# Performance work log

Measured on AMD Instinct MI355X. Metric: run time of the kernel, lower is better.

Reference implementation:

```python
import jax, jax.numpy as jnp
import numpy as np

NH = 8    # num_heads
HD = 64   # head_dim
EPS = 1e-6


def setup_inputs() -> dict:
    key = jax.random.key(0)
    ks = jax.random.split(key, 8)
    B, N, D = 16, 3136, 512
    x = jax.random.normal(ks[0], (B, N, D), jnp.float32)
    Wq = jax.random.normal(ks[1], (D, D), jnp.float32) * 0.02
    Wkv = jax.random.normal(ks[2], (D, 2 * D), jnp.float32) * 0.02
    pos_enc = jax.random.normal(ks[3], (1, N, D), jnp.float32) * 0.02
    # depthwise conv: fan_out = k*k*out/groups = 25
    dwc_w = jax.random.normal(ks[4], (HD, 1, 5, 5), jnp.float32) * np.sqrt(2.0 / 25.0).astype(np.float32)
    dwc_b = jnp.zeros((HD,), jnp.float32)
    Wp = jax.random.normal(ks[5], (D, D), jnp.float32) * 0.02
    bp = jnp.zeros((D,), jnp.float32)
    return {"x": x, "Wq": Wq, "Wkv": Wkv, "pos_enc": pos_enc,
            "dwc_w": dwc_w, "dwc_b": dwc_b, "Wp": Wp, "bp": bp,
            "H": 56, "W": 56}


def reference(x, Wq, Wkv, pos_enc, dwc_w, dwc_b, Wp, bp, H, W):
    B, N, D = x.shape
    # projections (qkv_bias=False)
    q = jax.nn.relu(x @ Wq)                       # ReLU feature map on q
    kv = x @ Wkv                                  # [B, N, 2D]
    k = jax.nn.relu(kv[..., :D] + pos_enc)        # pos enc added before ReLU kernel
    v = kv[..., D:]
    # split heads: b n (h c) -> b h n c
    qh = q.reshape(B, N, NH, HD).transpose(0, 2, 1, 3)
    kh = k.reshape(B, N, NH, HD).transpose(0, 2, 1, 3)
    vh = v.reshape(B, N, NH, HD).transpose(0, 2, 1, 3)
    # linear attention: normalization and KV context
    k_sum = kh.sum(axis=2)                                        # [B, NH, HD]
    d_inv = 1.0 / (jnp.einsum('bhnd,bhd->bhn', qh, k_sum) + EPS)  # [B, NH, N]
    ctx = jnp.einsum('bhmd,bhme->bhde', kh, vh)                   # [B, NH, HD, HD]
    attn = jnp.einsum('bhnd,bhde->bhne', qh, ctx) * d_inv[..., None]
    # depthwise conv positional mixing on v (N == H*W)
    fmap = vh.reshape(B * NH, H, W, HD).transpose(0, 3, 1, 2)     # [(b h), c, H, W]
    dwc = jax.lax.conv_general_dilated(
        fmap, dwc_w, window_strides=(1, 1), padding='SAME',
        feature_group_count=HD,
        dimension_numbers=('NCHW', 'OIHW', 'NCHW')) + dwc_b[None, :, None, None]
    dwc = dwc.transpose(0, 2, 3, 1).reshape(B, NH, N, HD)
    # NOTE: original torch code reshapes ((b h), n, c) -> (B, N, D) directly
    # (NOT the inverse rearrange); reproduce that exact flat reshape.
    out = (attn + dwc).reshape(B, N, D)
    return out @ Wp + bp
```

## Files before the change

kernel.cpp:

```cpp
#include <hip/hip_runtime.h>

__device__ __forceinline__ float b2f(ushort u) {
    union { float f; unsigned int i; } w; w.i = ((unsigned int)u) << 16; return w.f;
}
__device__ __forceinline__ ushort f2b(float f) {
    union { float f; unsigned int i; } w; w.f = f;
    unsigned int lsb = (w.i >> 16) & 1u;
    w.i += 0x7fffu + lsb;
    return (ushort)(w.i >> 16);
}

typedef __bf16 bf16x8 __attribute__((ext_vector_type(8)));
typedef float floatx4 __attribute__((ext_vector_type(4)));

__device__ __forceinline__ void async_copy16(ushort* lds_base, const ushort* gptr) {
    __builtin_amdgcn_global_load_lds(
        (const __attribute__((address_space(1))) unsigned int*)gptr,
        (__attribute__((address_space(3))) unsigned int*)lds_base,
        16, 0, 0);
}

#define BATCH 16
#define NTOK  3136
#define NHEAD 8
#define HDIM  64
#define HSP   56
#define MROWS (BATCH * NTOK)
#define KDIM  512

__global__ __launch_bounds__(256) void detect_dtype(const ushort* __restrict__ x,
                                                    int* __restrict__ flag)
{
    __shared__ int s;
    if (threadIdx.x == 0) s = 0;
    __syncthreads();
    int bad = 0;
    for (int i = threadIdx.x; i < 4096; i += 256) {
        int e = (x[i] >> 7) & 0xFF;
        if (e >= 0x90) bad = 1;
    }
    if (bad) s = 1;
    __syncthreads();
    if (threadIdx.x == 0) flag[0] = s;
}

__global__ __launch_bounds__(256) void convert_x(
    const void* __restrict__ x, const int* __restrict__ flag,
    ushort* __restrict__ xbf)
{
    size_t t = (size_t)blockIdx.x * 256 + threadIdx.x;
    if (flag[0]) {
        const float* xf = (const float*)x + t * 8;
        float4 f0 = *(const float4*)xf;
        float4 f1 = *(const float4*)(xf + 4);
        ushort o[8] = { f2b(f0.x), f2b(f0.y), f2b(f0.z), f2b(f0.w),
                        f2b(f1.x), f2b(f1.y), f2b(f1.z), f2b(f1.w) };
        *(uint4*)(xbf + t * 8) = *(const uint4*)o;
    } else {
        *(uint4*)(xbf + t * 8) = *((const uint4*)x + t);
    }
}

__global__ __launch_bounds__(256) void prep_weights(
    const void* __restrict__ Wq, const void* __restrict__ Wkv,
    const void* __restrict__ Wp, const int* __restrict__ flag,
    ushort* __restrict__ WqkvT, ushort* __restrict__ WpT)
{
    bool f32 = flag[0] != 0;
    int idx = blockIdx.x * 256 + threadIdx.x;
    int kk = idx & 511;
    int n  = idx >> 9;
    if (n < 1536) {
        ushort val;
        if (n < 512)
            val = f32 ? f2b(((const float*)Wq)[kk * 512 + n])
                      : ((const ushort*)Wq)[kk * 512 + n];
        else
            val = f32 ? f2b(((const float*)Wkv)[kk * 1024 + (n - 512)])
                      : ((const ushort*)Wkv)[kk * 1024 + (n - 512)];
        WqkvT[n * 512 + kk] = val;
    } else {
        int n2 = n - 1536;
        WpT[n2 * 512 + kk] = f32 ? f2b(((const float*)Wp)[kk * 512 + n2])
                                 : ((const ushort*)Wp)[kk * 512 + n2];
    }
}

__global__ __launch_bounds__(256) void prep_dwc(
    const void* __restrict__ dwc_w, const void* __restrict__ dwc_b,
    const int* __restrict__ flag, float* __restrict__ wT)
{
    bool f32 = flag[0] != 0;
    for (int i = threadIdx.x; i < 1600; i += 256) {
        int e = i / 25, tap = i % 25;
        float w = f32 ? ((const float*)dwc_w)[i] : b2f(((const ushort*)dwc_w)[i]);
        wT[tap * 64 + e] = w;
    }
    if (threadIdx.x < 64) {
        float b = f32 ? ((const float*)dwc_b)[threadIdx.x]
                      : b2f(((const ushort*)dwc_b)[threadIdx.x]);
        wT[1600 + threadIdx.x] = b;
    }
}

__device__ __forceinline__ int swz(int r) { return (r ^ (r >> 2)) & 3; }

#define VMWAIT(N) asm volatile("s_waitcnt vmcnt(" #N ")" ::: "memory")

__global__ __launch_bounds__(512, 2) void gemm256_bt(
    const ushort* __restrict__ A, const ushort* __restrict__ Bt,
    int mode, const int* __restrict__ flag,
    const void* __restrict__ pos_enc, const void* __restrict__ bias,
    void* __restrict__ out0, ushort* __restrict__ out1, ushort* __restrict__ out2,
    int ntn)
{
    __shared__ ushort smem[65536];

    const bool f32 = flag[0] != 0;
    const int tid = threadIdx.x;
    const int lam = tid & 63;
    const int w   = tid >> 6;
    const int wm  = w >> 2;
    const int wn  = w & 3;
    const int g    = lam >> 4;
    const int mrow = lam & 15;
    const int m7   = mrow & 7;

    const int nwg = gridDim.x;
    const int q8  = nwg >> 3;
    const int bid = blockIdx.x;
    const int fid = (bid & 7) * q8 + (bid >> 3);
    const int tm = fid / ntn, tn = fid - tm * ntn;
    const int m0 = tm * 256, n0 = tn * 256;

    const int srow = w * 16 + (lam >> 3);
    const int scol = 8 * ((lam & 7) ^ (lam >> 3));
    const ushort* gA0 = A  + (size_t)(m0 +       srow) * KDIM + scol;
    const ushort* gA1 = A  + (size_t)(m0 + 128 + srow) * KDIM + scol;
    const ushort* gB0 = Bt + (size_t)(n0 +       srow) * KDIM + scol;
    const ushort* gB1 = Bt + (size_t)(n0 + 128 + srow) * KDIM + scol;

    const int aoff = (wm * 64 + mrow) * 64;
    const int boff = (wn * 32 + mrow) * 64;
    const int kx0 = 8 * (g ^ m7);
    const int kx1 = 8 * ((4 + g) ^ m7);

    floatx4 acc[8][4];
    #pragma unroll
    for (int i = 0; i < 8; i++)
        #pragma unroll
        for (int j = 0; j < 4; j++) acc[i][j] = (floatx4)0.f;

    bf16x8 a[4][2], bfr[2][2];

#define SA(p,h) (((p)*2+(h))*8192)
#define SB(p,h) (32768 + ((p)*2+(h))*8192)
#define STAGE(gp, slot, koff) do { \
    async_copy16(smem + (slot) + w*1024,       (gp) + (koff)); \
    async_copy16(smem + (slot) + w*1024 + 512, (gp) + 4096 + (koff)); } while (0)

    auto LDA_HALF = [&](int h, int p) {
        const ushort* ab = smem + SA(p,h) + aoff;
        #pragma unroll
        for (int q = 0; q < 4; ++q) {
            a[q][0] = *(const bf16x8*)(ab + q*1024 + kx0);
            a[q][1] = *(const bf16x8*)(ab + q*1024 + kx1);
        }
    };
    auto LDB_HALF = [&](int h, int p) {
        const ushort* bb = smem + SB(p,h) + boff;
        #pragma unroll
        for (int nq = 0; nq < 2; ++nq) {
            bfr[nq][0] = *(const bf16x8*)(bb + nq*1024 + kx0);
            bfr[nq][1] = *(const bf16x8*)(bb + nq*1024 + kx1);
        }
    };

#define PH_SYNC() do { __builtin_amdgcn_s_barrier(); \
    asm volatile("s_waitcnt lgkmcnt(0)" ::: "memory"); \
    __builtin_amdgcn_sched_barrier(0); } while (0)

#define MFMA_QUAD(MH, NH) do { \
    __builtin_amdgcn_s_setprio(1); \
    _Pragma("unroll") \
    for (int q = 0; q < 4; ++q) { \
        _Pragma("unroll") \
        for (int nq = 0; nq < 2; ++nq) { \
            acc[(MH)*4+q][(NH)*2+nq] = __builtin_amdgcn_mfma_f32_16x16x32_bf16( \
                a[q][0], bfr[nq][0], acc[(MH)*4+q][(NH)*2+nq], 0, 0, 0); \
            acc[(MH)*4+q][(NH)*2+nq] = __builtin_amdgcn_mfma_f32_16x16x32_bf16( \
                a[q][1], bfr[nq][1], acc[(MH)*4+q][(NH)*2+nq], 0, 0, 0); \
        } } \
    __builtin_amdgcn_s_setprio(0); } while (0)

    STAGE(gA0, SA(0,0), 0);
    STAGE(gB0, SB(0,0), 0);
    STAGE(gB1, SB(0,1), 0);
    STAGE(gA1, SA(0,1), 0);
    VMWAIT(4);
    __builtin_amdgcn_s_barrier();

    for (int kt = 0; kt < 7; ++kt) {
        const int p = kt & 1, np = p ^ 1;
        const int ko = (kt + 1) * 64;
        LDA_HALF(0, p); LDB_HALF(0, p);
        STAGE(gA0, SA(np,0), ko);
        VMWAIT(4);
        PH_SYNC();
        MFMA_QUAD(0, 0);
        LDB_HALF(1, p);
        STAGE(gB0, SB(np,0), ko);
        VMWAIT(4);
        PH_SYNC();
        MFMA_QUAD(0, 1);
        LDA_HALF(1, p);
        STAGE(gB1, SB(np,1), ko);
        PH_SYNC();
        MFMA_QUAD(1, 1);
        LDB_HALF(0, p);
        STAGE(gA1, SA(np,1), ko);
        VMWAIT(4);
        PH_SYNC();
        MFMA_QUAD(1, 0);
    }
    {
        LDA_HALF(0, 1); LDB_HALF(0, 1);
        VMWAIT(2);
        PH_SYNC();
        MFMA_QUAD(0, 0);
        LDB_HALF(1, 1);
        VMWAIT(0);
        PH_SYNC();
        MFMA_QUAD(0, 1);
        LDA_HALF(1, 1);
        PH_SYNC();
        MFMA_QUAD(1, 1);
        LDB_HALF(0, 1);
        PH_SYNC();
        MFMA_QUAD(1, 0);
    }

    float* lf = (float*)smem;
    const int e0 = (lam & 7) * 8;
    #pragma unroll
    for (int h = 0; h < 2; ++h) {
        __syncthreads();
        #pragma unroll
        for (int q = 0; q < 4; ++q)
            #pragma unroll
            for (int ni = 0; ni < 4; ++ni)
                #pragma unroll
                for (int rr = 0; rr < 4; ++rr) {
                    int r = wm*64 + q*16 + g*4 + rr;
                    int c = (ni>>1)*128 + wn*32 + (ni&1)*16 + mrow;
                    lf[r*256 + (c ^ ((r&7)<<2))] = acc[h*4+q][ni][rr];
                }
        __syncthreads();
        #pragma unroll
        for (int rh = 0; rh < 2; ++rh) {
            const int rl = w*16 + (lam>>3) + rh*8;
            const int rg = m0 + h*128 + rl;
            const int bb = rg / NTOK;
            const int nn = rg - bb*NTOK;
            const int xr = (rl & 7) << 2;
            const float* lrow = lf + rl*256;
            #pragma unroll
            for (int cb = 0; cb < 4; ++cb) {
                const int c0 = cb*64 + e0;
                float4 v0 = *(const float4*)(lrow + ((c0    ) ^ xr));
                float4 v1 = *(const float4*)(lrow + ((c0 + 4) ^ xr));
                float vv[8] = {v0.x, v0.y, v0.z, v0.w, v1.x, v1.y, v1.z, v1.w};
                const int colg = n0 + c0;
                if (mode == 1) {
                    if (f32) {
                        float ob[8];
                        #pragma unroll
                        for (int j = 0; j < 8; j++)
                            ob[j] = vv[j] + ((const float*)bias)[colg + j];
                        float* o = (float*)out0 + (size_t)rg * 512 + colg;
                        *(float4*)o       = *(const float4*)&ob[0];
                        *(float4*)(o + 4) = *(const float4*)&ob[4];
                    } else {
                        ushort t8[8];
                        #pragma unroll
                        for (int j = 0; j < 8; j++)
                            t8[j] = f2b(vv[j] + b2f(((const ushort*)bias)[colg + j]));
                        *(uint4*)((ushort*)out0 + (size_t)rg * 512 + colg) = *(const uint4*)t8;
                    }
                } else {
                    const int tz = colg >> 9;
                    const size_t oadr =
                        (((size_t)bb * 8 + ((colg >> 6) & 7)) * NTOK + nn) * 64 + (colg & 63);
                    ushort t8[8];
                    if (tz == 0) {
                        #pragma unroll
                        for (int j = 0; j < 8; j++) t8[j] = f2b(fmaxf(vv[j], 0.f));
                        *(uint4*)((ushort*)out0 + oadr) = *(const uint4*)t8;
                    } else if (tz == 1) {
                        const int d0 = colg - 512;
                        #pragma unroll
                        for (int j = 0; j < 8; j++) {
                            float pe = f32 ? ((const float*)pos_enc)[(size_t)nn*512 + d0 + j]
                                           : b2f(((const ushort*)pos_enc)[(size_t)nn*512 + d0 + j]);
                            t8[j] = f2b(fmaxf(vv[j] + pe, 0.f));
                        }
                        *(uint4*)(out1 + oadr) = *(const uint4*)t8;
                    } else {
                        #pragma unroll
                        for (int j = 0; j < 8; j++) t8[j] = f2b(vv[j]);
                        *(uint4*)(out2 + oadr) = *(const uint4*)t8;
                    }
                }
            }
        }
    }
#undef SA
#undef SB
#undef STAGE
#undef PH_SYNC
#undef MFMA_QUAD
}

#define SPLITS 7
#define NPER   (NTOK / SPLITS)

__global__ __launch_bounds__(256) void ctx_ksum(
    const ushort* __restrict__ kbuf, const ushort* __restrict__ vbuf,
    float* __restrict__ ctx, float* __restrict__ ksum)
{
    __shared__ ushort kT[64 * 32];
    __shared__ ushort vT[64 * 32];
    __shared__ float ks4[256];
    int bh = blockIdx.x, sp = blockIdx.y;
    int tid = threadIdx.x;
    int lane = tid & 63, wave = tid >> 6;
    int mrow = lane & 15, g = lane >> 4;
    int r = tid & 31, cblk = tid >> 5;
    size_t base = ((size_t)bh * NTOK + sp * NPER) * 64;

    floatx4 acc[4];
    #pragma unroll
    for (int c = 0; c < 4; c++) acc[c] = (floatx4)0.f;
    float kpart = 0.f;
    int kd = tid >> 2, kq = tid & 3;

    for (int nc = 0; nc < NPER; nc += 32) {
        uint4 ku = *(const uint4*)(kbuf + base + (size_t)(nc + r) * 64 + cblk * 8);
        uint4 vu = *(const uint4*)(vbuf + base + (size_t)(nc + r) * 64 + cblk * 8);
        __syncthreads();
        const ushort* kp = (const ushort*)&ku;
        const ushort* vp = (const ushort*)&vu;
        #pragma unroll
        for (int j = 0; j < 8; j++) {
            int d = cblk * 8 + j;
            int blk = (r >> 3) ^ swz(d);
            kT[d * 32 + blk * 8 + (r & 7)] = kp[j];
            vT[d * 32 + blk * 8 + (r & 7)] = vp[j];
        }
        __syncthreads();
        {
            const ushort* p = &kT[kd * 32 + kq * 8];
            #pragma unroll
            for (int j = 0; j < 8; j++) kpart += b2f(p[j]);
        }
        int dr = wave * 16 + mrow;
        bf16x8 af = *(const bf16x8*)&kT[dr * 32 + (g ^ swz(dr)) * 8];
        #pragma unroll
        for (int c = 0; c < 4; c++) {
            int er = c * 16 + mrow;
            bf16x8 bf = *(const bf16x8*)&vT[er * 32 + (g ^ swz(er)) * 8];
            acc[c] = __builtin_amdgcn_mfma_f32_16x16x32_bf16(af, bf, acc[c], 0, 0, 0);
        }
    }
    #pragma unroll
    for (int c = 0; c < 4; c++)
        #pragma unroll
        for (int rr = 0; rr < 4; rr++) {
            int d = wave * 16 + g * 4 + rr;
            int e = c * 16 + mrow;
            atomicAdd(&ctx[bh * 4096 + d * 64 + e], acc[c][rr]);
        }
    ks4[tid] = kpart;
    __syncthreads();
    if (tid < 64) {
        float s = ks4[tid * 4] + ks4[tid * 4 + 1] + ks4[tid * 4 + 2] + ks4[tid * 4 + 3];
        atomicAdd(&ksum[bh * 64 + tid], s);
    }
}

__global__ __launch_bounds__(256) void attn_kernel(
    const ushort* __restrict__ q, const float* __restrict__ ctx,
    const float* __restrict__ ksum, ushort* __restrict__ ybuf)
{
    __shared__ float smem[4352];
    ushort* ctxT = (ushort*)smem;
    float* sout = smem;
    int bh = blockIdx.x, cg = blockIdx.y;
    int tid = threadIdx.x;
    int lane = tid & 63, wave = tid >> 6;
    int mrow = lane & 15, g = lane >> 4;

    for (int i = tid; i < 640; i += 256) {
        int e = i >> 3, blk = i & 7;
        ushort tmp[8];
        #pragma unroll
        for (int j = 0; j < 8; j++) {
            int d = blk * 8 + j;
            float v = 0.f;
            if (e < 64) v = ctx[bh * 4096 + d * 64 + e];
            else if (e == 64) v = ksum[bh * 64 + d];
            tmp[j] = f2b(v);
        }
        *(uint4*)&ctxT[e * 64 + (blk ^ (e & 7)) * 8] = *(const uint4*)tmp;
    }
    __syncthreads();

    bf16x8 bfr[2][5];
    #pragma unroll
    for (int kt = 0; kt < 2; kt++)
        #pragma unroll
        for (int c = 0; c < 5; c++) {
            int e = c * 16 + mrow;
            bfr[kt][c] = *(const bf16x8*)&ctxT[e * 64 + ((kt * 4 + g) ^ (e & 7)) * 8];
        }

    int token4 = tid >> 2, seg = tid & 3;
    for (int cc = 0; cc < 7; cc++) {
        int n0 = (cg * 7 + cc) * 64;
        floatx4 acc[5];
        #pragma unroll
        for (int c = 0; c < 5; c++) acc[c] = (floatx4)0.f;
        size_t qrow = ((size_t)bh * NTOK + n0 + wave * 16 + mrow) * 64;
        #pragma unroll
        for (int kt = 0; kt < 2; kt++) {
            bf16x8 af = *(const bf16x8*)(q + qrow + kt * 32 + g * 8);
            #pragma unroll
            for (int c = 0; c < 5; c++)
                acc[c] = __builtin_amdgcn_mfma_f32_16x16x32_bf16(af, bfr[kt][c], acc[c], 0, 0, 0);
        }
        __syncthreads();
        #pragma unroll
        for (int c = 0; c < 4; c++)
            #pragma unroll
            for (int rr = 0; rr < 4; rr++)
                sout[(wave * 16 + g * 4 + rr) * 68 + c * 16 + mrow] = acc[c][rr];
        if (mrow == 0) {
            #pragma unroll
            for (int rr = 0; rr < 4; rr++)
                sout[(wave * 16 + g * 4 + rr) * 68 + 64] = acc[4][rr];
        }
        __syncthreads();
        float dinv = 1.0f / (sout[token4 * 68 + 64] + 1e-6f);
        const float* sp = &sout[token4 * 68 + seg * 16];
        ushort res[16];
        #pragma unroll
        for (int j = 0; j < 16; j++) res[j] = f2b(sp[j] * dinv);
        ushort* o = ybuf + ((size_t)bh * NTOK + n0 + token4) * 64 + seg * 16;
        *(uint4*)o = *(const uint4*)res;
        *(uint4*)(o + 8) = *(const uint4*)(res + 8);
    }
}

__global__ __launch_bounds__(256) void dwc_add(
    const ushort* __restrict__ v, const float* __restrict__ wT,
    ushort* __restrict__ ybuf)
{
    __shared__ float wls[1664];
    for (int i = threadIdx.x; i < 1664; i += 256) wls[i] = wT[i];
    __syncthreads();

    int t = blockIdx.x * 256 + threadIdx.x;
    int eg = (t & 7) * 8;
    int r = t >> 3;
    int n  = r % NTOK;
    int bh = r / NTOK;
    int y = n / HSP, x = n % HSP;

    float acc[8];
    #pragma unroll
    for (int j = 0; j < 8; j++) acc[j] = wls[1600 + eg + j];

    const ushort* vb = v + (size_t)bh * NTOK * 64 + eg;
    #pragma unroll
    for (int dy = 0; dy < 5; ++dy) {
        int yy = y + dy - 2;
        if (yy < 0 || yy >= HSP) continue;
        #pragma unroll
        for (int dx = 0; dx < 5; ++dx) {
            int xx = x + dx - 2;
            if (xx < 0 || xx >= HSP) continue;
            uint4 u = *(const uint4*)(vb + (size_t)(yy * HSP + xx) * 64);
            const ushort* up = (const ushort*)&u;
            const float* wp = &wls[(dy * 5 + dx) * 64 + eg];
            #pragma unroll
            for (int j = 0; j < 8; j++) acc[j] += wp[j] * b2f(up[j]);
        }
    }
    size_t o = (size_t)r * 64 + eg;
    uint4 yo = *(const uint4*)(ybuf + o);
    const ushort* yp = (const ushort*)&yo;
    ushort res[8];
    #pragma unroll
    for (int j = 0; j < 8; j++) res[j] = f2b(acc[j] + b2f(yp[j]));
    *(uint4*)(ybuf + o) = *(const uint4*)res;
}

extern "C" void kernel_launch(void* const* d_in, const int* in_sizes, int n_in,
                              void* d_out, int out_size, void* d_ws, size_t ws_size,
                              hipStream_t stream) {
    const void* x    = d_in[0];
    const void* Wq   = d_in[1];
    const void* Wkv  = d_in[2];
    const void* pos  = d_in[3];
    const void* dwcw = d_in[4];
    const void* dwcb = d_in[5];
    const void* Wp   = d_in[6];
    const void* bp   = d_in[7];

    char* ws = (char*)d_ws;
    const size_t SZ_BIG = 51380224;
    int*    flag   = (int*)(ws + 0);
    ushort* WqkvT  = (ushort*)(ws + 4096);
    ushort* WpT    = (ushort*)(ws + 4096 + 1572864);
    float*  wTdwc  = (float*)(ws + 2101248);
    float*  ctx    = (float*)(ws + 2107904);
    float*  ksum   = (float*)(ws + 4205056);
    ushort* qbuf   = (ushort*)(ws + 4237824);
    ushort* kbuf   = (ushort*)(ws + 4237824 + SZ_BIG);
    ushort* vbuf   = (ushort*)(ws + 4237824 + 2 * SZ_BIG);
    ushort* xbf = (ushort*)d_out;

    detect_dtype<<<1, 256, 0, stream>>>((const ushort*)x, flag);
    hipMemsetAsync(ctx, 0, 2097152 + 32768, stream);

    prep_weights<<<4096, 256, 0, stream>>>(Wq, Wkv, Wp, flag, WqkvT, WpT);
    prep_dwc<<<1, 256, 0, stream>>>(dwcw, dwcb, flag, wTdwc);
    convert_x<<<12544, 256, 0, stream>>>(x, flag, xbf);

    gemm256_bt<<<dim3(196 * 6), 512, 0, stream>>>(
        xbf, WqkvT, 0, flag, pos, nullptr, qbuf, kbuf, vbuf, 6);

    ctx_ksum<<<dim3(128, SPLITS), 256, 0, stream>>>(kbuf, vbuf, ctx, ksum);

    attn_kernel<<<dim3(128, 7), 256, 0, stream>>>(qbuf, ctx, ksum, kbuf);

    dwc_add<<<12544, 256, 0, stream>>>(vbuf, wTdwc, kbuf);

    gemm256_bt<<<dim3(196 * 2), 512, 0, stream>>>(
        kbuf, WpT, 1, flag, nullptr, bp, d_out, nullptr, nullptr, 2);
}
```

Baseline: 538.5 us.

## Shrink GEMM K-tile to 32 with simple double buffer and halved LDS

Rewrites the 256x256 bf16 GEMM main loop to use K-steps of 32 instead of 64. It uses a plain two-stage double buffer in place of the four-phase interleaved half-tile schedule. LDS drops from 128KB to 64KB and launch bounds ask for 4 blocks per SM to raise occupancy. The epilogue is restaged in four 64-row passes to fit the smaller LDS. This trades more barriers and iterations, plus fewer MFMAs per sync, for possible extra occupancy, which the large accumulator register count may not actually allow.

```diff
diff --git a/kernel.cpp b/kernel.cpp
--- a/kernel.cpp
+++ b/kernel.cpp
@@ -106,15 +106,17 @@
 __device__ __forceinline__ int swz(int r) { return (r ^ (r >> 2)) & 3; }
 
 #define VMWAIT(N) asm volatile("s_waitcnt vmcnt(" #N ")" ::: "memory")
-
-__global__ __launch_bounds__(512, 2) void gemm256_bt(
+#define LGKM0()   do { asm volatile("s_waitcnt lgkmcnt(0)" ::: "memory"); \
+                       __builtin_amdgcn_sched_barrier(0); } while (0)
+
+__global__ __launch_bounds__(512, 4) void gemm256_bt(
     const ushort* __restrict__ A, const ushort* __restrict__ Bt,
     int mode, const int* __restrict__ flag,
     const void* __restrict__ pos_enc, const void* __restrict__ bias,
     void* __restrict__ out0, ushort* __restrict__ out1, ushort* __restrict__ out2,
     int ntn)
 {
-    __shared__ ushort smem[65536];
+    __shared__ ushort smem[32768];
 
     const bool f32 = flag[0] != 0;
     const int tid = threadIdx.x;
@@ -124,7 +126,6 @@
     const int wn  = w & 3;
     const int g    = lam >> 4;
     const int mrow = lam & 15;
-    const int m7   = mrow & 7;
 
     const int nwg = gridDim.x;
     const int q8  = nwg >> 3;
@@ -133,17 +134,15 @@
     const int tm = fid / ntn, tn = fid - tm * ntn;
     const int m0 = tm * 256, n0 = tn * 256;
 
-    const int srow = w * 16 + (lam >> 3);
-    const int scol = 8 * ((lam & 7) ^ (lam >> 3));
-    const ushort* gA0 = A  + (size_t)(m0 +       srow) * KDIM + scol;
-    const ushort* gA1 = A  + (size_t)(m0 + 128 + srow) * KDIM + scol;
-    const ushort* gB0 = Bt + (size_t)(n0 +       srow) * KDIM + scol;
-    const ushort* gB1 = Bt + (size_t)(n0 + 128 + srow) * KDIM + scol;
-
-    const int aoff = (wm * 64 + mrow) * 64;
-    const int boff = (wn * 32 + mrow) * 64;
-    const int kx0 = 8 * (g ^ m7);
-    const int kx1 = 8 * ((4 + g) ^ m7);
+    const int srow  = w * 32 + (lam >> 2);
+    const int scol8 = 8 * ((lam & 3) ^ ((lam >> 3) & 3));
+    const ushort* gA = A  + (size_t)(m0 + srow) * KDIM + scol8;
+    const ushort* gB = Bt + (size_t)(n0 + srow) * KDIM + scol8;
+
+    const int axor = ((g ^ ((mrow >> 1) & 3)) << 3);
+    const int arow0 = (wm * 64 + mrow) * 32 + axor;
+    const int arow1 = (128 + wm * 64 + mrow) * 32 + axor;
+    const int brow  = (wn * 32 + mrow) * 32 + axor;
 
     floatx4 acc[8][4];
     #pragma unroll
@@ -151,165 +150,132 @@
         #pragma unroll
         for (int j = 0; j < 4; j++) acc[i][j] = (floatx4)0.f;
 
-    bf16x8 a[4][2], bfr[2][2];
-
-#define SA(p,h) (((p)*2+(h))*8192)
-#define SB(p,h) (32768 + ((p)*2+(h))*8192)
-#define STAGE(gp, slot, koff) do { \
-    async_copy16(smem + (slot) + w*1024,       (gp) + (koff)); \
-    async_copy16(smem + (slot) + w*1024 + 512, (gp) + 4096 + (koff)); } while (0)
-
-    auto LDA_HALF = [&](int h, int p) {
-        const ushort* ab = smem + SA(p,h) + aoff;
-        #pragma unroll
-        for (int q = 0; q < 4; ++q) {
-            a[q][0] = *(const bf16x8*)(ab + q*1024 + kx0);
-            a[q][1] = *(const bf16x8*)(ab + q*1024 + kx1);
-        }
-    };
-    auto LDB_HALF = [&](int h, int p) {
-        const ushort* bb = smem + SB(p,h) + boff;
-        #pragma unroll
-        for (int nq = 0; nq < 2; ++nq) {
-            bfr[nq][0] = *(const bf16x8*)(bb + nq*1024 + kx0);
-            bfr[nq][1] = *(const bf16x8*)(bb + nq*1024 + kx1);
-        }
-    };
-
-#define PH_SYNC() do { __builtin_amdgcn_s_barrier(); \
-    asm volatile("s_waitcnt lgkmcnt(0)" ::: "memory"); \
-    __builtin_amdgcn_sched_barrier(0); } while (0)
-
-#define MFMA_QUAD(MH, NH) do { \
-    __builtin_amdgcn_s_setprio(1); \
-    _Pragma("unroll") \
-    for (int q = 0; q < 4; ++q) { \
-        _Pragma("unroll") \
-        for (int nq = 0; nq < 2; ++nq) { \
-            acc[(MH)*4+q][(NH)*2+nq] = __builtin_amdgcn_mfma_f32_16x16x32_bf16( \
-                a[q][0], bfr[nq][0], acc[(MH)*4+q][(NH)*2+nq], 0, 0, 0); \
-            acc[(MH)*4+q][(NH)*2+nq] = __builtin_amdgcn_mfma_f32_16x16x32_bf16( \
-                a[q][1], bfr[nq][1], acc[(MH)*4+q][(NH)*2+nq], 0, 0, 0); \
-        } } \
-    __builtin_amdgcn_s_setprio(0); } while (0)
-
-    STAGE(gA0, SA(0,0), 0);
-    STAGE(gB0, SB(0,0), 0);
-    STAGE(gB1, SB(0,1), 0);
-    STAGE(gA1, SA(0,1), 0);
-    VMWAIT(4);
-    __builtin_amdgcn_s_barrier();
-
-    for (int kt = 0; kt < 7; ++kt) {
-        const int p = kt & 1, np = p ^ 1;
-        const int ko = (kt + 1) * 64;
-        LDA_HALF(0, p); LDB_HALF(0, p);
-        STAGE(gA0, SA(np,0), ko);
-        VMWAIT(4);
-        PH_SYNC();
-        MFMA_QUAD(0, 0);
-        LDB_HALF(1, p);
-        STAGE(gB0, SB(np,0), ko);
-        VMWAIT(4);
-        PH_SYNC();
-        MFMA_QUAD(0, 1);
-        LDA_HALF(1, p);
-        STAGE(gB1, SB(np,1), ko);
-        PH_SYNC();
-        MFMA_QUAD(1, 1);
-        LDB_HALF(0, p);
-        STAGE(gA1, SA(np,1), ko);
-        VMWAIT(4);
-        PH_SYNC();
-        MFMA_QUAD(1, 0);
-    }
-    {
-        LDA_HALF(0, 1); LDB_HALF(0, 1);
-        VMWAIT(2);
-        PH_SYNC();
-        MFMA_QUAD(0, 0);
-        LDB_HALF(1, 1);
-        VMWAIT(0);
-        PH_SYNC();
-        MFMA_QUAD(0, 1);
-        LDA_HALF(1, 1);
-        PH_SYNC();
-        MFMA_QUAD(1, 1);
-        LDB_HALF(0, 1);
-        PH_SYNC();
-        MFMA_QUAD(1, 0);
+#define SA(p) ((p) * 8192)
+#define SB(p) (16384 + (p) * 8192)
+#define STAGE(p, kt1) do { \
+    const int ko = (kt1) * 32; \
+    async_copy16(smem + SA(p) + w * 1024,       gA + ko); \
+    async_copy16(smem + SA(p) + w * 1024 + 512, gA + 16 * KDIM + ko); \
+    async_copy16(smem + SB(p) + w * 1024,       gB + ko); \
+    async_copy16(smem + SB(p) + w * 1024 + 512, gB + 16 * KDIM + ko); } while (0)
+
+    STAGE(0, 0);
+
+    #pragma unroll
+    for (int kt = 0; kt < 16; ++kt) {
+        const int p = kt & 1;
+        if (kt < 15) {
+            STAGE(p ^ 1, kt + 1);
+            VMWAIT(4);
+        } else {
+            VMWAIT(0);
+        }
+        __builtin_amdgcn_s_barrier();
+        __builtin_amdgcn_sched_barrier(0);
+
+        const ushort* sa = smem + SA(p);
+        const ushort* sb = smem + SB(p);
+
+        bf16x8 a0[4], bb[4];
+        #pragma unroll
+        for (int q = 0; q < 4; ++q) a0[q] = *(const bf16x8*)(sa + arow0 + q * 512);
+        #pragma unroll
+        for (int j = 0; j < 4; ++j)
+            bb[j] = *(const bf16x8*)(sb + brow + (j >> 1) * 4096 + (j & 1) * 512);
+        LGKM0();
+        __builtin_amdgcn_s_setprio(1);
+        #pragma unroll
+        for (int q = 0; q < 4; ++q)
+            #pragma unroll
+            for (int j = 0; j < 4; ++j)
+                acc[q][j] = __builtin_amdgcn_mfma_f32_16x16x32_bf16(
+                    a0[q], bb[j], acc[q][j], 0, 0, 0);
+        __builtin_amdgcn_s_setprio(0);
+
+        bf16x8 a1[4];
+        #pragma unroll
+        for (int q = 0; q < 4; ++q) a1[q] = *(const bf16x8*)(sa + arow1 + q * 512);
+        LGKM0();
+        __builtin_amdgcn_s_barrier();
+        __builtin_amdgcn_s_setprio(1);
+        #pragma unroll
+        for (int q = 0; q < 4; ++q)
+            #pragma unroll
+            for (int j = 0; j < 4; ++j)
+                acc[4 + q][j] = __builtin_amdgcn_mfma_f32_16x16x32_bf16(
+                    a1[q], bb[j], acc[4 + q][j], 0, 0, 0);
+        __builtin_amdgcn_s_setprio(0);
     }
 
     float* lf = (float*)smem;
-    const int e0 = (lam & 7) * 8;
-    #pragma unroll
-    for (int h = 0; h < 2; ++h) {
+    const int rl  = tid >> 3;
+    const int e0  = (tid & 7) * 8;
+    const int xrr = (rl & 7) << 2;
+    #pragma unroll
+    for (int h4 = 0; h4 < 4; ++h4) {
         __syncthreads();
-        #pragma unroll
-        for (int q = 0; q < 4; ++q)
-            #pragma unroll
-            for (int ni = 0; ni < 4; ++ni)
+        if (wm == (h4 & 1)) {
+            #pragma unroll
+            for (int q = 0; q < 4; ++q)
                 #pragma unroll
-                for (int rr = 0; rr < 4; ++rr) {
-                    int r = wm*64 + q*16 + g*4 + rr;
-                    int c = (ni>>1)*128 + wn*32 + (ni&1)*16 + mrow;
-                    lf[r*256 + (c ^ ((r&7)<<2))] = acc[h*4+q][ni][rr];
+                for (int j = 0; j < 4; ++j)
+                    #pragma unroll
+                    for (int rr = 0; rr < 4; ++rr) {
+                        int r = q * 16 + g * 4 + rr;
+                        int c = (j >> 1) * 128 + wn * 32 + (j & 1) * 16 + mrow;
+                        lf[r * 256 + (c ^ ((r & 7) << 2))] = acc[(h4 >> 1) * 4 + q][j][rr];
+                    }
+        }
+        __syncthreads();
+        const int rg = m0 + h4 * 64 + rl;
+        const int bb2 = rg / NTOK;
+        const int nn  = rg - bb2 * NTOK;
+        const float* lrow = lf + rl * 256;
+        #pragma unroll
+        for (int cb = 0; cb < 4; ++cb) {
+            const int c0 = cb * 64 + e0;
+            float4 v0 = *(const float4*)(lrow + ((c0    ) ^ xrr));
+            float4 v1 = *(const float4*)(lrow + ((c0 + 4) ^ xrr));
+            float vv[8] = {v0.x, v0.y, v0.z, v0.w, v1.x, v1.y, v1.z, v1.w};
+            const int colg = n0 + c0;
+            if (mode == 1) {
+                if (f32) {
+                    float ob[8];
+                    #pragma unroll
+                    for (int j = 0; j < 8; j++)
+                        ob[j] = vv[j] + ((const float*)bias)[colg + j];
+                    float* o = (float*)out0 + (size_t)rg * 512 + colg;
+                    *(float4*)o       = *(const float4*)&ob[0];
+                    *(float4*)(o + 4) = *(const float4*)&ob[4];
+                } else {
+                    ushort t8[8];
+                    #pragma unroll
+                    for (int j = 0; j < 8; j++)
+                        t8[j] = f2b(vv[j] + b2f(((const ushort*)bias)[colg + j]));
+                    *(uint4*)((ushort*)out0 + (size_t)rg * 512 + colg) = *(const uint4*)t8;
                 }
-        __syncthreads();
-        #pragma unroll
-        for (int rh = 0; rh < 2; ++rh) {
-            const int rl = w*16 + (lam>>3) + rh*8;
-            const int rg = m0 + h*128 + rl;
-            const int bb = rg / NTOK;
-            const int nn = rg - bb*NTOK;
-            const int xr = (rl & 7) << 2;
-            const float* lrow = lf + rl*256;
-            #pragma unroll
-            for (int cb = 0; cb < 4; ++cb) {
-                const int c0 = cb*64 + e0;
-                float4 v0 = *(const float4*)(lrow + ((c0    ) ^ xr));
-                float4 v1 = *(const float4*)(lrow + ((c0 + 4) ^ xr));
-                float vv[8] = {v0.x, v0.y, v0.z, v0.w, v1.x, v1.y, v1.z, v1.w};
-                const int colg = n0 + c0;
-                if (mode == 1) {
-                    if (f32) {
-                        float ob[8];
-                        #pragma unroll
-                        for (int j = 0; j < 8; j++)
-                            ob[j] = vv[j] + ((const float*)bias)[colg + j];
-                        float* o = (float*)out0 + (size_t)rg * 512 + colg;
-                        *(float4*)o       = *(const float4*)&ob[0];
-                        *(float4*)(o + 4) = *(const float4*)&ob[4];
-                    } else {
-                        ushort t8[8];
-                        #pragma unroll
-                        for (int j = 0; j < 8; j++)
-                            t8[j] = f2b(vv[j] + b2f(((const ushort*)bias)[colg + j]));
-                        *(uint4*)((ushort*)out0 + (size_t)rg * 512 + colg) = *(const uint4*)t8;
+            } else {
+                const int tz = colg >> 9;
+                const size_t oadr =
+                    (((size_t)bb2 * 8 + ((colg >> 6) & 7)) * NTOK + nn) * 64 + (colg & 63);
+                ushort t8[8];
+                if (tz == 0) {
+                    #pragma unroll
+                    for (int j = 0; j < 8; j++) t8[j] = f2b(fmaxf(vv[j], 0.f));
+                    *(uint4*)((ushort*)out0 + oadr) = *(const uint4*)t8;
+                } else if (tz == 1) {
+                    const int d0 = colg - 512;
+                    #pragma unroll
+                    for (int j = 0; j < 8; j++) {
+                        float pe = f32 ? ((const float*)pos_enc)[(size_t)nn * 512 + d0 + j]
+                                       : b2f(((const ushort*)pos_enc)[(size_t)nn * 512 + d0 + j]);
+                        t8[j] = f2b(fmaxf(vv[j] + pe, 0.f));
                     }
+                    *(uint4*)(out1 + oadr) = *(const uint4*)t8;
                 } else {
-                    const int tz = colg >> 9;
-                    const size_t oadr =
-                        (((size_t)bb * 8 + ((colg >> 6) & 7)) * NTOK + nn) * 64 + (colg & 63);
-                    ushort t8[8];
-                    if (tz == 0) {
-                        #pragma unroll
-                        for (int j = 0; j < 8; j++) t8[j] = f2b(fmaxf(vv[j], 0.f));
-                        *(uint4*)((ushort*)out0 + oadr) = *(const uint4*)t8;
-                    } else if (tz == 1) {
-                        const int d0 = colg - 512;
-                        #pragma unroll
-                        for (int j = 0; j < 8; j++) {
-                            float pe = f32 ? ((const float*)pos_enc)[(size_t)nn*512 + d0 + j]
-                                           : b2f(((const ushort*)pos_enc)[(size_t)nn*512 + d0 + j]);
-                            t8[j] = f2b(fmaxf(vv[j] + pe, 0.f));
-                        }
-                        *(uint4*)(out1 + oadr) = *(const uint4*)t8;
-                    } else {
-                        #pragma unroll
-                        for (int j = 0; j < 8; j++) t8[j] = f2b(vv[j]);
-                        *(uint4*)(out2 + oadr) = *(const uint4*)t8;
-                    }
+                    #pragma unroll
+                    for (int j = 0; j < 8; j++) t8[j] = f2b(vv[j]);
+                    *(uint4*)(out2 + oadr) = *(const uint4*)t8;
                 }
             }
         }
@@ -317,8 +283,6 @@
 #undef SA
 #undef SB
 #undef STAGE
-#undef PH_SYNC
-#undef MFMA_QUAD
 }
 
 #define SPLITS 7
```

Result: slower. 1.379 ms (+156.1%).
